# Kernel tuning notes

Measured on AMD Instinct MI355X. Metric: run time of the kernel, lower is better.

## Reference

```python
import jax, jax.numpy as jnp
import numpy as np

B, T, C, E = 16, 1024, 256, 512
NUM_CENTER = [512, 256, 128]
NUM_NNS = [16, 32, 64]
BN_EPS = 1e-5


def _fps(pts, K):
    # farthest point sampling, deterministic start at index 0. pts: [B,N,3] -> [B,K] int32
    N = pts.shape[1]
    def one(p):
        def step(carry, _):
            d, cur = carry
            dist = jnp.sum((p - p[cur]) ** 2, axis=-1)
            d = jnp.minimum(d, dist)
            nxt = jnp.argmax(d).astype(jnp.int32)
            return (d, nxt), cur
        init = (jnp.full((N,), jnp.inf, p.dtype), jnp.int32(0))
        _, idxs = jax.lax.scan(step, init, None, length=K)
        return idxs
    return jax.vmap(one)(pts)


def _knn(q, t, k):
    # k nearest neighbors of each query q [B,Tq,3] among targets t [B,Tt,3] -> [B,Tq,k]
    d2 = (jnp.sum(q * q, -1)[:, :, None] + jnp.sum(t * t, -1)[:, None, :]
          - 2.0 * jnp.einsum('bqc,btc->bqt', q, t))
    _, idx = jax.lax.top_k(-d2, k)
    return idx


def _gather(x, idx):
    # x [B,N,C], idx [B,M] -> [B,M,C]
    return jax.vmap(lambda xb, ib: xb[ib])(x, idx)


def _knn_gather(x, idx):
    # x [B,N,C], idx [B,M,K] -> [B,M,K,C]
    return jax.vmap(lambda xb, ib: xb[ib])(x, idx)


def _bn(x, g, b):
    # training-mode BatchNorm1d over leading (batch) dim of [N,C]
    m = jnp.mean(x, axis=0)
    v = jnp.mean((x - m) ** 2, axis=0)
    return (x - m) * jax.lax.rsqrt(v + BN_EPS) * g + b


def reference(tokens, centers, lrfs, wq, wkv, mlp_w1, mlp_b1, mlp_w2, mlp_b2,
              bn1_g, bn1_b, bn2_g, bn2_b, att_w1, att_b1, att_w2, att_b2,
              emb_w, emb_b, embn_g, embn_b):
    Bq, Tt, Cd = tokens.shape
    centers_target = centers
    lrfs_target = lrfs.reshape(Bq, Tt, 9)
    tokens_target = tokens
    T_target = Tt
    for i in range(len(NUM_CENTER)):
        Tq = NUM_CENTER[i]
        k = NUM_NNS[i]
        rep_idx = _fps(centers_target, Tq)                      # [B,Tq]
        centers_query = _gather(centers_target, rep_idx)        # [B,Tq,3]
        lrfs_query = _gather(lrfs_target, rep_idx)              # [B,Tq,9]
        tokens_query = _gather(tokens_target, rep_idx)          # [B,Tq,C]
        nn_idx = _knn(centers_query, centers_target, k)         # [B,Tq,k]
        skip = tokens_query.reshape(Bq * Tq, Cd)
        if i > 0:
            t = jnp.concatenate([tokens_query, tokens_target], axis=1)
            t = _bn(t.reshape(Bq * (Tq + T_target), Cd), bn1_g[i], bn1_b[i])
            t = t.reshape(Bq, Tq + T_target, Cd)
            tokens_query, tokens_target = t[:, :Tq, :], t[:, Tq:, :]
        Q = tokens_query @ wq[i]                                # [B,Tq,C]
        KV = tokens_target @ wkv[i]                             # [B,Tt,2C]
        Kf, Vf = KV[..., :Cd], KV[..., Cd:]
        Kn = _knn_gather(Kf, nn_idx).reshape(Bq * Tq, k, Cd)
        Vn = _knn_gather(Vf, nn_idx).reshape(Bq * Tq, k, Cd)
        Qf = Q.reshape(Bq * Tq, Cd)
        # vector self-attention: elementwise Q-K diff -> MLP -> softmax over neighbors
        diff = Qf[:, None, :] - Kn                              # [B*Tq,k,C]
        sim = jax.nn.relu(diff @ att_w1[i] + att_b1[i]) @ att_w2[i] + att_b2[i]
        A = jax.nn.softmax(sim, axis=1)
        tq = jnp.sum(A * Vn, axis=1)                            # [B*Tq,C]
        tq = tq + skip
        skip2 = tq
        tq = _bn(tq, bn2_g[i], bn2_b[i])
        tq = jax.nn.relu(tq @ mlp_w1[i] + mlp_b1[i]) @ mlp_w2[i] + mlp_b2[i]
        tq = tq + skip2
        T_target = Tq
        centers_target = centers_query
        lrfs_target = lrfs_query
        tokens_target = tq.reshape(Bq, Tq, Cd)
    g = jnp.mean(tokens_target, axis=1)                         # [B,C]
    g = jax.nn.relu(_bn(g @ emb_w + emb_b, embn_g, embn_b))     # [B,E]
    # ksparse: keep top-64 activations per row
    vals, _ = jax.lax.top_k(g, 64)
    thr = vals[:, -1:]
    g = jnp.where(g >= thr, g, 0.0)
    n = jnp.maximum(jnp.linalg.norm(g, axis=1, keepdims=True), 1e-12)
    return g / n


def setup_inputs() -> dict:
    key = jax.random.key(0)
    ks = jax.random.split(key, 10)
    s = 0.05
    return {
        'tokens': jax.random.normal(ks[0], (B, T, C), jnp.float32),
        'centers': jax.random.normal(ks[1], (B, T, 3), jnp.float32),
        'lrfs': jax.random.normal(ks[2], (B, T, 3, 3), jnp.float32),
        'wq': jax.random.normal(ks[3], (3, C, C), jnp.float32) * s,
        'wkv': jax.random.normal(ks[4], (3, C, 2 * C), jnp.float32) * s,
        'mlp_w1': jax.random.normal(ks[5], (3, C, 2 * C), jnp.float32) * s,
        'mlp_b1': jnp.zeros((3, 2 * C), jnp.float32),
        'mlp_w2': jax.random.normal(ks[6], (3, 2 * C, C), jnp.float32) * s,
        'mlp_b2': jnp.zeros((3, C), jnp.float32),
        'bn1_g': jnp.ones((3, C), jnp.float32),
        'bn1_b': jnp.zeros((3, C), jnp.float32),
        'bn2_g': jnp.ones((3, C), jnp.float32),
        'bn2_b': jnp.zeros((3, C), jnp.float32),
        'att_w1': jax.random.normal(ks[7], (3, C, C), jnp.float32) * s,
        'att_b1': jnp.zeros((3, C), jnp.float32),
        'att_w2': jax.random.normal(ks[8], (3, C, C), jnp.float32) * s,
        'att_b2': jnp.zeros((3, C), jnp.float32),
        'emb_w': jax.random.normal(ks[9], (C, E), jnp.float32) * s,
        'emb_b': jnp.zeros((E,), jnp.float32),
        'embn_g': jnp.ones((E,), jnp.float32),
        'embn_b': jnp.zeros((E,), jnp.float32),
    }
```

## Files before the change

### kernel.cpp

```cpp
#include <hip/hip_runtime.h>
#include <cstdint>
#include <cmath>

static constexpr int BB = 16;
static constexpr int TT0 = 1024;
static constexpr int CC = 256;
static constexpr int EE = 512;

typedef __bf16 bf16x8 __attribute__((ext_vector_type(8)));
typedef float  f32x4  __attribute__((ext_vector_type(4)));

template <int NPL>
__device__ void fps_body(float4* sp, const float* __restrict__ ctr,
                         int Tt, int Ksel, int* __restrict__ rep,
                         int b, int lane)
{
  const float* base = ctr + (size_t)b * Tt * 3;
  float x[NPL], y[NPL], z[NPL], d[NPL];
  #pragma unroll
  for (int j = 0; j < NPL; ++j) {
    int idx = lane * NPL + j;
    x[j] = base[idx * 3 + 0];
    y[j] = base[idx * 3 + 1];
    z[j] = base[idx * 3 + 2];
    d[j] = INFINITY;
    sp[idx] = make_float4(x[j], y[j], z[j], 0.f);
  }
  int cur = 0;
  for (int s = 0; s < Ksel; ++s) {
    if (lane == 0) rep[b * Ksel + s] = cur;
    float4 cpt = sp[cur];
    unsigned long long key = 0ull;
    #pragma unroll
    for (int j = 0; j < NPL; ++j) {
      float dx = __fsub_rn(x[j], cpt.x);
      float dy = __fsub_rn(y[j], cpt.y);
      float dz = __fsub_rn(z[j], cpt.z);
      float dist = __fadd_rn(__fadd_rn(__fmul_rn(dx, dx), __fmul_rn(dy, dy)),
                             __fmul_rn(dz, dz));
      float nd = fminf(d[j], dist);
      d[j] = nd;
      unsigned long long kj =
          ((unsigned long long)__float_as_uint(nd) << 32) |
          (unsigned)(0xFFFFFFFFu - (unsigned)(lane * NPL + j));
      key = (kj > key) ? kj : key;
    }
    float ld = __uint_as_float((unsigned)(key >> 32));
    float rm = ld;
    {
      int t;
      t = __builtin_amdgcn_mov_dpp(__float_as_int(rm), 0x121, 0xf, 0xf, false);
      rm = fmaxf(rm, __int_as_float(t));
      t = __builtin_amdgcn_mov_dpp(__float_as_int(rm), 0x122, 0xf, 0xf, false);
      rm = fmaxf(rm, __int_as_float(t));
      t = __builtin_amdgcn_mov_dpp(__float_as_int(rm), 0x124, 0xf, 0xf, false);
      rm = fmaxf(rm, __int_as_float(t));
      t = __builtin_amdgcn_mov_dpp(__float_as_int(rm), 0x128, 0xf, 0xf, false);
      rm = fmaxf(rm, __int_as_float(t));
    }
    float r0 = __uint_as_float((unsigned)__builtin_amdgcn_readlane(__float_as_int(rm), 0));
    float r1 = __uint_as_float((unsigned)__builtin_amdgcn_readlane(__float_as_int(rm), 16));
    float r2 = __uint_as_float((unsigned)__builtin_amdgcn_readlane(__float_as_int(rm), 32));
    float r3 = __uint_as_float((unsigned)__builtin_amdgcn_readlane(__float_as_int(rm), 48));
    float gm = fmaxf(fmaxf(r0, r1), fmaxf(r2, r3));
    unsigned long long mask = __ballot(ld == gm);
    int wl = __ffsll(mask) - 1;
    unsigned lowkey = (unsigned)__builtin_amdgcn_readlane((int)(unsigned)key, wl);
    cur = (int)(0xFFFFFFFFu - lowkey);
  }
}

template <int NPL2>
__global__ __launch_bounds__(256) void knn_wave_kernel(
    const float* __restrict__ cq, const float* __restrict__ ct,
    int Tq, int Tt, int Kn, int* __restrict__ nn)
{
  int wid = threadIdx.x >> 6, lane = threadIdx.x & 63;
  int r = blockIdx.x * 4 + wid;
  int b = r / Tq;
  const float* tb = ct + (size_t)b * Tt * 3;
  float qx = cq[(size_t)r * 3 + 0];
  float qy = cq[(size_t)r * 3 + 1];
  float qz = cq[(size_t)r * 3 + 2];
  float sq = __fadd_rn(__fadd_rn(__fmul_rn(qx, qx), __fmul_rn(qy, qy)),
                       __fmul_rn(qz, qz));
  unsigned long long key[NPL2];
  #pragma unroll
  for (int j = 0; j < NPL2; ++j) {
    int t = lane * NPL2 + j;
    float tx = tb[t * 3 + 0], ty = tb[t * 3 + 1], tz = tb[t * 3 + 2];
    float st = __fadd_rn(__fadd_rn(__fmul_rn(tx, tx), __fmul_rn(ty, ty)),
                         __fmul_rn(tz, tz));
    float dot = __fadd_rn(__fadd_rn(__fmul_rn(qx, tx), __fmul_rn(qy, ty)),
                          __fmul_rn(qz, tz));
    float d2 = __fsub_rn(__fadd_rn(sq, st), __fmul_rn(2.0f, dot));
    unsigned ub = __float_as_uint(d2);
    ub ^= (ub >> 31) ? 0xFFFFFFFFu : 0x80000000u;
    key[j] = ((unsigned long long)ub << 32) | (unsigned)t;
  }
  for (int k = 0; k < Kn; ++k) {
    unsigned long long lmin = ~0ull;
    #pragma unroll
    for (int j = 0; j < NPL2; ++j) lmin = (key[j] < lmin) ? key[j] : lmin;
    unsigned md = (unsigned)(lmin >> 32);
    unsigned rm = md;
    {
      unsigned t;
      t = (unsigned)__builtin_amdgcn_mov_dpp((int)rm, 0x121, 0xf, 0xf, false);
      rm = (t < rm) ? t : rm;
      t = (unsigned)__builtin_amdgcn_mov_dpp((int)rm, 0x122, 0xf, 0xf, false);
      rm = (t < rm) ? t : rm;
      t = (unsigned)__builtin_amdgcn_mov_dpp((int)rm, 0x124, 0xf, 0xf, false);
      rm = (t < rm) ? t : rm;
      t = (unsigned)__builtin_amdgcn_mov_dpp((int)rm, 0x128, 0xf, 0xf, false);
      rm = (t < rm) ? t : rm;
    }
    unsigned r0 = (unsigned)__builtin_amdgcn_readlane((int)rm, 0);
    unsigned r1 = (unsigned)__builtin_amdgcn_readlane((int)rm, 16);
    unsigned r2 = (unsigned)__builtin_amdgcn_readlane((int)rm, 32);
    unsigned r3 = (unsigned)__builtin_amdgcn_readlane((int)rm, 48);
    unsigned g01 = (r0 < r1) ? r0 : r1;
    unsigned g23 = (r2 < r3) ? r2 : r3;
    unsigned gmin = (g01 < g23) ? g01 : g23;
    unsigned long long mask = __ballot(md == gmin);
    int wl = __ffsll(mask) - 1;
    int wt = __builtin_amdgcn_readlane((int)(unsigned)lmin, wl);
    if (lane == 0) nn[(size_t)r * Kn + k] = wt;
    #pragma unroll
    for (int j = 0; j < NPL2; ++j)
      if (lane * NPL2 + j == wt) key[j] = ~0ull;
  }
}

__global__ void gather_rows_kernel(
    const float* __restrict__ src, const int* __restrict__ idx,
    float* __restrict__ dst, int Tq, int Tt, int D, int total)
{
  int i = blockIdx.x * blockDim.x + threadIdx.x;
  if (i >= total) return;
  int d = i % D;
  int q = (i / D) % Tq;
  int b = i / (D * Tq);
  int s = idx[b * Tq + q];
  dst[i] = src[((size_t)b * Tt + s) * D + d];
}

__global__ __launch_bounds__(256) void bn_stats_kernel(
    const float* __restrict__ x1, int R1, const float* __restrict__ x2, int R2,
    float* __restrict__ part, int nch)
{
  int c = threadIdx.x;
  int chunk = blockIdx.x;
  int R = R1 + R2;
  int per = (R + nch - 1) / nch;
  int r0 = chunk * per;
  int r1 = min(r0 + per, R);
  float s = 0.f, ss = 0.f;
  for (int r = r0; r < r1; ++r) {
    float v = (r < R1) ? x1[(size_t)r * 256 + c] : x2[(size_t)(r - R1) * 256 + c];
    s += v;
    ss = fmaf(v, v, ss);
  }
  part[(size_t)chunk * 512 + c] = s;
  part[(size_t)chunk * 512 + 256 + c] = ss;
}

__global__ __launch_bounds__(256) void bn_finalize_kernel(
    const float* __restrict__ part, int nch, int R,
    float* __restrict__ mean, float* __restrict__ rstd)
{
  int c = threadIdx.x;
  float s = 0.f, ss = 0.f;
  for (int k = 0; k < nch; ++k) {
    s += part[(size_t)k * 512 + c];
    ss += part[(size_t)k * 512 + 256 + c];
  }
  float m = s / (float)R;
  float v = ss / (float)R - m * m;
  if (v < 0.f) v = 0.f;
  mean[c] = m;
  rstd[c] = rsqrtf(v + 1e-5f);
}

__global__ __launch_bounds__(256) void gemm_kernel(
    const float* __restrict__ A, int lda,
    const float* __restrict__ W, int ldw,
    const float* __restrict__ bias, const float* __restrict__ resid,
    float* __restrict__ out, int M, int N, int K, int relu)
{
  __shared__ float As[32][68];
  __shared__ float Bs[32][68];
  int bm = blockIdx.y * 64;
  int bn = blockIdx.x * 64;
  int tid = threadIdx.x;
  int tx = tid & 15, ty = tid >> 4;
  int arow = tid >> 3;
  int ak = (tid & 7) * 4;
  int wk = tid >> 4;
  int wn = (tid & 15) * 4;
  float acc[4][4] = {{0.f}};
  for (int k0 = 0; k0 < K; k0 += 32) {
    #pragma unroll
    for (int h = 0; h < 2; ++h) {
      int row = bm + arow + h * 32;
      float4 a = (row < M)
          ? *(const float4*)&A[(size_t)row * lda + k0 + ak]
          : make_float4(0.f, 0.f, 0.f, 0.f);
      As[ak + 0][arow + h * 32] = a.x;
      As[ak + 1][arow + h * 32] = a.y;
      As[ak + 2][arow + h * 32] = a.z;
      As[ak + 3][arow + h * 32] = a.w;
    }
    #pragma unroll
    for (int h = 0; h < 2; ++h) {
      int krow = k0 + wk + h * 16;
      *(float4*)&Bs[wk + h * 16][wn] =
          *(const float4*)&W[(size_t)krow * ldw + bn + wn];
    }
    __syncthreads();
    #pragma unroll
    for (int k = 0; k < 32; ++k) {
      float4 a = *(const float4*)&As[k][ty * 4];
      float4 b = *(const float4*)&Bs[k][tx * 4];
      float av[4] = {a.x, a.y, a.z, a.w};
      float bv[4] = {b.x, b.y, b.z, b.w};
      #pragma unroll
      for (int i = 0; i < 4; ++i)
        #pragma unroll
        for (int j = 0; j < 4; ++j)
          acc[i][j] = fmaf(av[i], bv[j], acc[i][j]);
    }
    __syncthreads();
  }
  #pragma unroll
  for (int i = 0; i < 4; ++i) {
    int m = bm + ty * 4 + i;
    if (m >= M) continue;
    #pragma unroll
    for (int j = 0; j < 4; ++j) {
      int n = bn + tx * 4 + j;
      float v = acc[i][j];
      if (bias) v += bias[n];
      if (relu) v = fmaxf(v, 0.f);
      if (resid) v += resid[(size_t)m * N + n];
      out[(size_t)m * N + n] = v;
    }
  }
}

__global__ __launch_bounds__(256) void gemm_fold_split_kernel(
    const float* __restrict__ A, int lda,
    const float* __restrict__ W, int ldw,
    __bf16* __restrict__ hi, __bf16* __restrict__ lo, int M, int N, int K)
{
  __shared__ float As[32][68];
  __shared__ float Bs[32][68];
  int bm = blockIdx.y * 64;
  int bn = blockIdx.x * 64;
  int tid = threadIdx.x;
  int tx = tid & 15, ty = tid >> 4;
  int arow = tid >> 3;
  int ak = (tid & 7) * 4;
  int wk = tid >> 4;
  int wn = (tid & 15) * 4;
  float acc[4][4] = {{0.f}};
  for (int k0 = 0; k0 < K; k0 += 32) {
    #pragma unroll
    for (int h = 0; h < 2; ++h) {
      int row = bm + arow + h * 32;
      float4 a = *(const float4*)&A[(size_t)row * lda + k0 + ak];
      As[ak + 0][arow + h * 32] = a.x;
      As[ak + 1][arow + h * 32] = a.y;
      As[ak + 2][arow + h * 32] = a.z;
      As[ak + 3][arow + h * 32] = a.w;
    }
    #pragma unroll
    for (int h = 0; h < 2; ++h) {
      int krow = k0 + wk + h * 16;
      *(float4*)&Bs[wk + h * 16][wn] =
          *(const float4*)&W[(size_t)krow * ldw + bn + wn];
    }
    __syncthreads();
    #pragma unroll
    for (int k = 0; k < 32; ++k) {
      float4 a = *(const float4*)&As[k][ty * 4];
      float4 b = *(const float4*)&Bs[k][tx * 4];
      float av[4] = {a.x, a.y, a.z, a.w};
      float bv[4] = {b.x, b.y, b.z, b.w};
      #pragma unroll
      for (int i = 0; i < 4; ++i)
        #pragma unroll
        for (int j = 0; j < 4; ++j)
          acc[i][j] = fmaf(av[i], bv[j], acc[i][j]);
    }
    __syncthreads();
  }
  #pragma unroll
  for (int i = 0; i < 4; ++i) {
    int m = bm + ty * 4 + i;
    #pragma unroll
    for (int j = 0; j < 4; ++j) {
      int n = bn + tx * 4 + j;
      float v = acc[i][j];
      __bf16 h = (__bf16)v;
      hi[(size_t)n * K + m] = h;
      lo[(size_t)n * K + m] = (__bf16)(v - (float)h);
    }
  }
}

__global__ void splitT_kernel(
    const float* __restrict__ src, int ldw, int K, int N,
    __bf16* __restrict__ hi, __bf16* __restrict__ lo, int total)
{
  int i = blockIdx.x * blockDim.x + threadIdx.x;
  if (i >= total) return;
  int n = i / K;
  int k = i - n * K;
  float v = src[(size_t)k * ldw + n];
  __bf16 h = (__bf16)v;
  hi[i] = h;
  lo[i] = (__bf16)(v - (float)h);
}

__global__ __launch_bounds__(256) void split_w2_kernel(
    const float* __restrict__ w2, __bf16* __restrict__ hi,
    __bf16* __restrict__ lo)
{
  int i = blockIdx.x * 256 + threadIdx.x;
  int s = i >> 16;
  int e = i & 65535;
  int cp = e >> 8;
  int cc = e & 255;
  float v = w2[((size_t)s << 16) + cc * 256 + cp];
  __bf16 h = (__bf16)v;
  hi[i] = h;
  lo[i] = (__bf16)(v - (float)h);
}

template <int NPL>
__global__ __launch_bounds__(256) void gemm_mfma_kernel(
    const float* __restrict__ A, int lda,
    const __bf16* __restrict__ WThi, const __bf16* __restrict__ WTlo,
    const float* __restrict__ bias, const float* __restrict__ resid,
    float* __restrict__ out, int M, int N, int K, int relu,
    const float* __restrict__ bnm, const float* __restrict__ bnr,
    const float* __restrict__ bng, const float* __restrict__ bnb,
    int nbx,
    const float* __restrict__ fps_ctr, int fps_Tt, int fps_Ksel,
    int* __restrict__ fps_rep)
{
  __shared__ __align__(16) float As[128 * 36];
  if ((int)blockIdx.x >= nbx) {
    if (fps_rep == nullptr || (int)blockIdx.y >= BB) return;
    if ((int)threadIdx.x >= 64) return;
    fps_body<NPL>((float4*)As, fps_ctr, fps_Tt, fps_Ksel, fps_rep,
                  blockIdx.y, threadIdx.x);
    return;
  }
  int bm = blockIdx.y * 128;
  int bn = blockIdx.x * 64;
  int tid = threadIdx.x;
  int w = tid >> 6, lane = tid & 63;
  int jl = lane & 15;
  int kg = lane >> 4;

  f32x4 acc[2][4];
  #pragma unroll
  for (int mt = 0; mt < 2; ++mt)
    #pragma unroll
    for (int nt = 0; nt < 4; ++nt) acc[mt][nt] = (f32x4){0.f, 0.f, 0.f, 0.f};

  for (int k0 = 0; k0 < K; k0 += 32) {
    #pragma unroll
    for (int f = 0; f < 4; ++f) {
      int fi = tid + f * 256;
      int row = fi >> 3, c4 = fi & 7;
      float4 v = *(const float4*)&A[(size_t)(bm + row) * lda + k0 + c4 * 4];
      if (bnm) {
        int kk = k0 + c4 * 4;
        float4 m4 = *(const float4*)&bnm[kk];
        float4 r4 = *(const float4*)&bnr[kk];
        float4 g4 = *(const float4*)&bng[kk];
        float4 b4 = *(const float4*)&bnb[kk];
        v.x = (v.x - m4.x) * r4.x * g4.x + b4.x;
        v.y = (v.y - m4.y) * r4.y * g4.y + b4.y;
        v.z = (v.z - m4.z) * r4.z * g4.z + b4.z;
        v.w = (v.w - m4.w) * r4.w * g4.w + b4.w;
      }
      *(float4*)&As[row * 36 + c4 * 4] = v;
    }
    __syncthreads();
    bf16x8 ahi[2], alo[2];
    #pragma unroll
    for (int mt = 0; mt < 2; ++mt) {
      int row = (w * 2 + mt) * 16 + jl;
      float4 a0 = *(const float4*)&As[row * 36 + kg * 8];
      float4 a1 = *(const float4*)&As[row * 36 + kg * 8 + 4];
      float hv[8] = {a0.x, a0.y, a0.z, a0.w, a1.x, a1.y, a1.z, a1.w};
      #pragma unroll
      for (int i = 0; i < 8; ++i) {
        __bf16 t0 = (__bf16)hv[i];
        ahi[mt][i] = t0;
        alo[mt][i] = (__bf16)(hv[i] - (float)t0);
      }
    }
    #pragma unroll
    for (int nt = 0; nt < 4; ++nt) {
      size_t boff = (size_t)(bn + nt * 16 + jl) * K + k0 + kg * 8;
      bf16x8 bhi = *(const bf16x8*)(WThi + boff);
      bf16x8 blo = *(const bf16x8*)(WTlo + boff);
      #pragma unroll
      for (int mt = 0; mt < 2; ++mt) {
        acc[mt][nt] = __builtin_amdgcn_mfma_f32_16x16x32_bf16(alo[mt], bhi, acc[mt][nt], 0, 0, 0);
        acc[mt][nt] = __builtin_amdgcn_mfma_f32_16x16x32_bf16(ahi[mt], blo, acc[mt][nt], 0, 0, 0);
        acc[mt][nt] = __builtin_amdgcn_mfma_f32_16x16x32_bf16(ahi[mt], bhi, acc[mt][nt], 0, 0, 0);
      }
    }
    __syncthreads();
  }
  #pragma unroll
  for (int mt = 0; mt < 2; ++mt)
    #pragma unroll
    for (int nt = 0; nt < 4; ++nt)
      #pragma unroll
      for (int qi = 0; qi < 4; ++qi) {
        int m = bm + (w * 2 + mt) * 16 + kg * 4 + qi;
        int n = bn + nt * 16 + jl;
        float v = acc[mt][nt][qi];
        if (bias) v += bias[n];
        if (relu) v = fmaxf(v, 0.f);
        if (resid) v += resid[(size_t)m * N + n];
        out[(size_t)m * N + n] = v;
      }
}

template <int KN, int NPL>
__global__ __launch_bounds__(256, 2) void attn5_kernel(
    const float* __restrict__ Qw, const float* __restrict__ KV,
    const int* __restrict__ nn,
    const float* __restrict__ b1, const __bf16* __restrict__ w2Thi,
    const __bf16* __restrict__ w2Tlo, const float* __restrict__ b2,
    const float* __restrict__ skip, float* __restrict__ out, int Tq, int Tt,
    int nbx,
    const float* __restrict__ fps_ctr, int fps_Tt, int fps_Ksel,
    int* __restrict__ fps_rep)
{
  constexpr int G  = 128 / KN;
  constexpr int GC = 64 / KN;
  constexpr int LD = 260;
  __shared__ __align__(16) float sim[64 * LD];
  __shared__ int nns[128];
  if ((int)blockIdx.x >= nbx) {
    if (fps_rep == nullptr) return;
    int fb = blockIdx.x - nbx;
    if (fb >= BB) return;
    if ((int)threadIdx.x >= 64) return;
    fps_body<NPL>((float4*)sim, fps_ctr, fps_Tt, fps_Ksel, fps_rep,
                  fb, threadIdx.x);
    return;
  }
  int r0 = blockIdx.x * G;
  int b = r0 / Tq;
  int tid = threadIdx.x;
  if (tid < 128) nns[tid] = nn[(size_t)r0 * KN + tid];
  __syncthreads();

  int w = tid >> 6, lane = tid & 63;
  int jl = lane & 15;
  int kg = lane >> 4;
  int nt0 = w * 4;
  const float* kvb = KV + (size_t)b * Tt * 512;

  f32x4 acc[8][4];
  #pragma unroll
  for (int m = 0; m < 8; ++m)
    #pragma unroll
    for (int n = 0; n < 4; ++n) acc[m][n] = (f32x4){0.f, 0.f, 0.f, 0.f};

  const float* qp[8];
  const float* kp[8];
  #pragma unroll
  for (int mt = 0; mt < 8; ++mt) {
    int jr = mt * 16 + jl;
    qp[mt] = Qw + (size_t)(r0 + jr / KN) * 256;
    kp[mt] = kvb + (size_t)nns[jr] * 512;
  }

  #pragma unroll
  for (int ks = 0; ks < 8; ++ks) {
    int c0 = ks * 32 + kg * 8;
    float4 b1a = *(const float4*)(b1 + c0);
    float4 b1b = *(const float4*)(b1 + c0 + 4);
    bf16x8 ahi[8], alo[8];
    #pragma unroll
    for (int mt = 0; mt < 8; ++mt) {
      float4 qa = *(const float4*)(qp[mt] + c0);
      float4 qb = *(const float4*)(qp[mt] + c0 + 4);
      float4 ka = *(const float4*)(kp[mt] + c0);
      float4 kb = *(const float4*)(kp[mt] + c0 + 4);
      float h[8];
      h[0] = fmaxf(qa.x - ka.x + b1a.x, 0.f);
      h[1] = fmaxf(qa.y - ka.y + b1a.y, 0.f);
      h[2] = fmaxf(qa.z - ka.z + b1a.z, 0.f);
      h[3] = fmaxf(qa.w - ka.w + b1a.w, 0.f);
      h[4] = fmaxf(qb.x - kb.x + b1b.x, 0.f);
      h[5] = fmaxf(qb.y - kb.y + b1b.y, 0.f);
      h[6] = fmaxf(qb.z - kb.z + b1b.z, 0.f);
      h[7] = fmaxf(qb.w - kb.w + b1b.w, 0.f);
      #pragma unroll
      for (int i = 0; i < 8; ++i) {
        __bf16 t0 = (__bf16)h[i];
        ahi[mt][i] = t0;
        alo[mt][i] = (__bf16)(h[i] - (float)t0);
      }
    }
    #pragma unroll
    for (int t = 0; t < 4; ++t) {
      size_t boff = (size_t)((nt0 + t) * 16 + jl) * 256 + c0;
      bf16x8 bhi = *(const bf16x8*)(w2Thi + boff);
      bf16x8 blo = *(const bf16x8*)(w2Tlo + boff);
      #pragma unroll
      for (int mt = 0; mt < 8; ++mt) {
        acc[mt][t] = __builtin_amdgcn_mfma_f32_16x16x32_bf16(alo[mt], bhi, acc[mt][t], 0, 0, 0);
        acc[mt][t] = __builtin_amdgcn_mfma_f32_16x16x32_bf16(ahi[mt], blo, acc[mt][t], 0, 0, 0);
        acc[mt][t] = __builtin_amdgcn_mfma_f32_16x16x32_bf16(ahi[mt], bhi, acc[mt][t], 0, 0, 0);
      }
    }
  }

  int c = tid;
  float bb2 = b2[c];
  const float* vbb = kvb + 256;
  #pragma unroll
  for (int ch = 0; ch < 2; ++ch) {
    if (ch) __syncthreads();
    #pragma unroll
    for (int m2 = 0; m2 < 4; ++m2) {
      int mt = ch * 4 + m2;
      #pragma unroll
      for (int t = 0; t < 4; ++t)
        #pragma unroll
        for (int qi = 0; qi < 4; ++qi)
          sim[(m2 * 16 + kg * 4 + qi) * LD + (nt0 + t) * 16 + jl] = acc[mt][t][qi];
    }
    __syncthreads();
    #pragma unroll
    for (int gg = 0; gg < GC; ++gg) {
      int jb_l = gg * KN;
      int jb_g = ch * 64 + gg * KN;
      float m = -INFINITY;
      #pragma unroll 8
      for (int jj = 0; jj < KN; ++jj)
        m = fmaxf(m, sim[(jb_l + jj) * LD + c] + bb2);
      float ssum = 0.f, o = 0.f;
      #pragma unroll 8
      for (int jj = 0; jj < KN; ++jj) {
        float e = expf(sim[(jb_l + jj) * LD + c] + bb2 - m);
        ssum += e;
        o = fmaf(e, vbb[(size_t)nns[jb_g + jj] * 512 + c], o);
      }
      int r = r0 + ch * GC + gg;
      out[(size_t)r * 256 + c] = o / ssum + skip[(size_t)r * 256 + c];
    }
  }
}

__global__ void gmean_kernel(const float* __restrict__ tok,
                             float* __restrict__ out, int Tt)
{
  int i = blockIdx.x * blockDim.x + threadIdx.x;
  if (i >= BB * CC) return;
  int b = i >> 8;
  int c = i & 255;
  float s = 0.f;
  for (int t = 0; t < Tt; ++t) s += tok[((size_t)b * Tt + t) * 256 + c];
  out[i] = s / (float)Tt;
}

__global__ void embbn_kernel(const float* __restrict__ x,
                             const float* __restrict__ g,
                             const float* __restrict__ bta,
                             float* __restrict__ y)
{
  int e = blockIdx.x * blockDim.x + threadIdx.x;
  if (e >= EE) return;
  float s = 0.f;
  for (int r = 0; r < BB; ++r) s += x[r * EE + e];
  float m = s / (float)BB;
  float vs = 0.f;
  for (int r = 0; r < BB; ++r) {
    float d = x[r * EE + e] - m;
    vs = fmaf(d, d, vs);
  }
  float rs = rsqrtf(vs / (float)BB + 1e-5f);
  for (int r = 0; r < BB; ++r) {
    float val = (x[r * EE + e] - m) * rs * g[e] + bta[e];
    y[r * EE + e] = fmaxf(val, 0.f);
  }
}

__global__ __launch_bounds__(256) void topk_norm_kernel(
    const float* __restrict__ gin, float* __restrict__ out)
{
  int b = blockIdx.x, tid = threadIdx.x, lane = tid & 63, wid = tid >> 6;
  __shared__ float vals[512];
  __shared__ float wv[4];
  __shared__ int wi[4];
  __shared__ float sh;
  float g0 = gin[b * 512 + tid];
  float g1 = gin[b * 512 + 256 + tid];
  vals[tid] = g0;
  vals[256 + tid] = g1;
  __syncthreads();
  for (int it = 0; it < 64; ++it) {
    float v = vals[tid];
    int ix = tid;
    float u = vals[256 + tid];
    if (u > v) { v = u; ix = 256 + tid; }
    #pragma unroll
    for (int off = 32; off > 0; off >>= 1) {
      float ov = __shfl_down(v, off);
      int oi = __shfl_down(ix, off);
      if (ov > v || (ov == v && oi < ix)) { v = ov; ix = oi; }
    }
    if (lane == 0) { wv[wid] = v; wi[wid] = ix; }
    __syncthreads();
    if (tid == 0) {
      float bv = wv[0]; int bi = wi[0];
      for (int w = 1; w < 4; ++w)
        if (wv[w] > bv || (wv[w] == bv && wi[w] < bi)) { bv = wv[w]; bi = wi[w]; }
      vals[bi] = -INFINITY;
      sh = bv;
    }
    __syncthreads();
  }
  float thr = sh;
  float m0 = (g0 >= thr) ? g0 : 0.f;
  float m1 = (g1 >= thr) ? g1 : 0.f;
  float ss = m0 * m0 + m1 * m1;
  #pragma unroll
  for (int off = 32; off > 0; off >>= 1) ss += __shfl_down(ss, off);
  if (lane == 0) wv[wid] = ss;
  __syncthreads();
  if (tid == 0) {
    float t = wv[0] + wv[1] + wv[2] + wv[3];
    sh = fmaxf(sqrtf(t), 1e-12f);
  }
  __syncthreads();
  float n = sh;
  out[b * 512 + tid] = m0 / n;
  out[b * 512 + 256 + tid] = m1 / n;
}

extern "C" void kernel_launch(void* const* d_in, const int* in_sizes, int n_in,
                              void* d_out, int out_size, void* d_ws, size_t ws_size,
                              hipStream_t stream)
{
  const float* tokens  = (const float*)d_in[0];
  const float* centers = (const float*)d_in[1];
  const float* wq      = (const float*)d_in[3];
  const float* wkv     = (const float*)d_in[4];
  const float* mlp_w1  = (const float*)d_in[5];
  const float* mlp_b1  = (const float*)d_in[6];
  const float* mlp_w2  = (const float*)d_in[7];
  const float* mlp_b2  = (const float*)d_in[8];
  const float* bn1_g   = (const float*)d_in[9];
  const float* bn1_b   = (const float*)d_in[10];
  const float* bn2_g   = (const float*)d_in[11];
  const float* bn2_b   = (const float*)d_in[12];
  const float* att_w1  = (const float*)d_in[13];
  const float* att_b1  = (const float*)d_in[14];
  const float* att_w2  = (const float*)d_in[15];
  const float* att_b2  = (const float*)d_in[16];
  const float* emb_w   = (const float*)d_in[17];
  const float* emb_b   = (const float*)d_in[18];
  const float* embn_g  = (const float*)d_in[19];
  const float* embn_b  = (const float*)d_in[20];
  (void)in_sizes; (void)n_in; (void)out_size; (void)ws_size;

  char* ws = (char*)d_ws;
  size_t off = 0;
  auto alloc = [&](size_t bytes) -> void* {
    void* p = ws + off;
    off += (bytes + 255) & ~(size_t)255;
    return p;
  };
  const size_t tokMax  = (size_t)BB * 512 * CC * 4;
  float* tokA     = (float*)alloc(tokMax);
  float* tokB     = (float*)alloc(tokMax);
  float* ctrA     = (float*)alloc((size_t)BB * 512 * 3 * 4);
  float* ctrB     = (float*)alloc((size_t)BB * 256 * 3 * 4);
  float* ctrC     = (float*)alloc((size_t)BB * 128 * 3 * 4);
  float* tokq_raw = (float*)alloc(tokMax);
  float* Qw1      = (float*)alloc(tokMax);
  float* KVbuf    = (float*)alloc((size_t)BB * 1024 * 512 * 4);
  float* tq1      = (float*)alloc(tokMax);
  float* mlph     = (float*)alloc((size_t)BB * 512 * 512 * 4);
  __bf16* w2Thi   = (__bf16*)alloc((size_t)3 * CC * CC * 2);
  __bf16* w2Tlo   = (__bf16*)alloc((size_t)3 * CC * CC * 2);
  __bf16* wfqThi  = (__bf16*)alloc((size_t)3 * CC * CC * 2);
  __bf16* wfqTlo  = (__bf16*)alloc((size_t)3 * CC * CC * 2);
  __bf16* wkvThi  = (__bf16*)alloc((size_t)3 * 512 * CC * 2);
  __bf16* wkvTlo  = (__bf16*)alloc((size_t)3 * 512 * CC * 2);
  __bf16* w1Thi   = (__bf16*)alloc((size_t)3 * CC * 512 * 2);
  __bf16* w1Tlo   = (__bf16*)alloc((size_t)3 * CC * 512 * 2);
  __bf16* wm2Thi  = (__bf16*)alloc((size_t)3 * 512 * CC * 2);
  __bf16* wm2Tlo  = (__bf16*)alloc((size_t)3 * 512 * CC * 2);
  int*   rep0     = (int*)alloc((size_t)BB * 512 * 4);
  int*   rep1     = (int*)alloc((size_t)BB * 256 * 4);
  int*   rep2     = (int*)alloc((size_t)BB * 128 * 4);
  int*   nnb      = (int*)alloc((size_t)BB * 512 * 64 * 4);
  float* bnpart   = (float*)alloc((size_t)64 * 512 * 4);
  float* bn1mean  = (float*)alloc(256 * 4);
  float* bn1rstd  = (float*)alloc(256 * 4);
  float* bn2mean  = (float*)alloc(256 * 4);
  float* bn2rstd  = (float*)alloc(256 * 4);
  float* gmeanb   = (float*)alloc((size_t)BB * CC * 4);
  float* gembb    = (float*)alloc((size_t)BB * EE * 4);
  float* grelub   = (float*)alloc((size_t)BB * EE * 4);

  const int NC[3] = {512, 256, 128};
  const int NN[3] = {16, 32, 64};
  int* reps[3] = {rep0, rep1, rep2};
  float* ctrq[3] = {ctrA, ctrB, ctrC};

  for (int i = 0; i < 3; ++i) {
    int t1 = CC * CC;
    gemm_fold_split_kernel<<<dim3(4, 4), 256, 0, stream>>>(
        wq + (size_t)i * CC * CC, CC, att_w1 + (size_t)i * CC * CC, CC,
        wfqThi + (size_t)i * t1, wfqTlo + (size_t)i * t1, CC, CC, CC);
    gemm_fold_split_kernel<<<dim3(4, 4), 256, 0, stream>>>(
        wkv + (size_t)i * CC * 512, 512, att_w1 + (size_t)i * CC * CC, CC,
        wkvThi + (size_t)i * 512 * CC, wkvTlo + (size_t)i * 512 * CC, CC, CC, CC);
    splitT_kernel<<<(t1 + 255) / 256, 256, 0, stream>>>(
        wkv + (size_t)i * CC * 512 + CC, 512, CC, CC,
        wkvThi + (size_t)i * 512 * CC + t1, wkvTlo + (size_t)i * 512 * CC + t1, t1);
    int t2 = CC * 512;
    splitT_kernel<<<(t2 + 255) / 256, 256, 0, stream>>>(
        mlp_w1 + (size_t)i * t2, 512, CC, 512,
        w1Thi + (size_t)i * t2, w1Tlo + (size_t)i * t2, t2);
    splitT_kernel<<<(t2 + 255) / 256, 256, 0, stream>>>(
        mlp_w2 + (size_t)i * t2, CC, 512, CC,
        wm2Thi + (size_t)i * t2, wm2Tlo + (size_t)i * t2, t2);
  }
  split_w2_kernel<<<3 * 65536 / 256, 256, 0, stream>>>(att_w2, w2Thi, w2Tlo);

  const float* cur_tok = tokens;
  const float* cur_ctr = centers;
  int curTt = TT0;
  float* tok_bufs[2] = {tokA, tokB};

  for (int i = 0; i < 3; ++i) {
    int Tq = NC[i], Kn = NN[i], Tt = curTt;
    float* ctr_q = ctrq[i];
    float* tok_next = tok_bufs[i & 1];
    int M = BB * Tq;
    int Mt = BB * Tt;
    int* rep = reps[i];

    const float *b1m = nullptr, *b1r = nullptr, *b1g = nullptr, *b1b = nullptr;

    if (i == 0) {
      gemm_mfma_kernel<16><<<dim3(512 / 64 + 1, Mt / 128), 256, 0, stream>>>(
          tokens, CC, wkvThi, wkvTlo, nullptr, nullptr, KVbuf,
          Mt, 512, CC, 0, nullptr, nullptr, nullptr, nullptr,
          512 / 64, centers, 1024, 512, rep0);
    }

    {
      int tot = BB * Tq * 3;
      gather_rows_kernel<<<(tot + 255) / 256, 256, 0, stream>>>(
          cur_ctr, rep, ctr_q, Tq, Tt, 3, tot);
    }
    {
      int tot = M * CC;
      gather_rows_kernel<<<(tot + 255) / 256, 256, 0, stream>>>(
          cur_tok, rep, tokq_raw, Tq, Tt, CC, tot);
    }
    if (Tt == 1024)
      knn_wave_kernel<16><<<M / 4, 256, 0, stream>>>(ctr_q, cur_ctr, Tq, Tt, Kn, nnb);
    else if (Tt == 512)
      knn_wave_kernel<8><<<M / 4, 256, 0, stream>>>(ctr_q, cur_ctr, Tq, Tt, Kn, nnb);
    else
      knn_wave_kernel<4><<<M / 4, 256, 0, stream>>>(ctr_q, cur_ctr, Tq, Tt, Kn, nnb);

    if (i > 0) {
      bn_stats_kernel<<<64, 256, 0, stream>>>(tokq_raw, M, cur_tok, Mt, bnpart, 64);
      bn_finalize_kernel<<<1, 256, 0, stream>>>(bnpart, 64, M + Mt, bn1mean, bn1rstd);
      b1m = bn1mean; b1r = bn1rstd; b1g = bn1_g + i * CC; b1b = bn1_b + i * CC;
      gemm_mfma_kernel<4><<<dim3(512 / 64, Mt / 128), 256, 0, stream>>>(
          cur_tok, CC, wkvThi + (size_t)i * 512 * CC, wkvTlo + (size_t)i * 512 * CC,
          nullptr, nullptr, KVbuf, Mt, 512, CC, 0, b1m, b1r, b1g, b1b,
          512 / 64, nullptr, 0, 0, nullptr);
    }

    gemm_mfma_kernel<4><<<dim3(CC / 64, M / 128), 256, 0, stream>>>(
        tokq_raw, CC, wfqThi + (size_t)i * CC * CC, wfqTlo + (size_t)i * CC * CC,
        nullptr, nullptr, Qw1, M, CC, CC, 0, b1m, b1r, b1g, b1b,
        CC / 64, nullptr, 0, 0, nullptr);

    if (Kn == 16)
      attn5_kernel<16, 8><<<dim3(M / 8 + 16), 256, 0, stream>>>(
          Qw1, KVbuf, nnb, att_b1 + i * CC,
          w2Thi + (size_t)i * CC * CC, w2Tlo + (size_t)i * CC * CC,
          att_b2 + i * CC, tokq_raw, tq1, Tq, Tt,
          M / 8, ctrA, 512, 256, rep1);
    else if (Kn == 32)
      attn5_kernel<32, 4><<<dim3(M / 4 + 16), 256, 0, stream>>>(
          Qw1, KVbuf, nnb, att_b1 + i * CC,
          w2Thi + (size_t)i * CC * CC, w2Tlo + (size_t)i * CC * CC,
          att_b2 + i * CC, tokq_raw, tq1, Tq, Tt,
          M / 4, ctrB, 256, 128, rep2);
    else
      attn5_kernel<64, 4><<<dim3(M / 2), 256, 0, stream>>>(
          Qw1, KVbuf, nnb, att_b1 + i * CC,
          w2Thi + (size_t)i * CC * CC, w2Tlo + (size_t)i * CC * CC,
          att_b2 + i * CC, tokq_raw, tq1, Tq, Tt,
          M / 2, nullptr, 0, 0, nullptr);

    bn_stats_kernel<<<64, 256, 0, stream>>>(tq1, M, tq1, 0, bnpart, 64);
    bn_finalize_kernel<<<1, 256, 0, stream>>>(bnpart, 64, M, bn2mean, bn2rstd);
    gemm_mfma_kernel<4><<<dim3(512 / 64, M / 128), 256, 0, stream>>>(
        tq1, CC, w1Thi + (size_t)i * CC * 512, w1Tlo + (size_t)i * CC * 512,
        mlp_b1 + i * 512, nullptr, mlph, M, 512, CC, 1,
        bn2mean, bn2rstd, bn2_g + i * CC, bn2_b + i * CC,
        512 / 64, nullptr, 0, 0, nullptr);
    gemm_mfma_kernel<4><<<dim3(CC / 64, M / 128), 256, 0, stream>>>(
        mlph, 512, wm2Thi + (size_t)i * 512 * CC, wm2Tlo + (size_t)i * 512 * CC,
        mlp_b2 + i * CC, tq1, tok_next, M, CC, 512, 0,
        nullptr, nullptr, nullptr, nullptr,
        CC / 64, nullptr, 0, 0, nullptr);

    cur_tok = tok_next;
    cur_ctr = ctr_q;
    curTt = Tq;
  }

  gmean_kernel<<<(BB * CC + 255) / 256, 256, 0, stream>>>(cur_tok, gmeanb, curTt);
  gemm_kernel<<<dim3(EE / 64, 1), 256, 0, stream>>>(
      gmeanb, CC, emb_w, EE, emb_b, nullptr, gembb, BB, EE, CC, 0);
  embbn_kernel<<<2, 256, 0, stream>>>(gembb, embn_g, embn_b, grelub);
  topk_norm_kernel<<<BB, 256, 0, stream>>>(grelub, (float*)d_out);
}
```

Baseline: 1.638 ms.

## Fuse stage-0 query projection into KV GEMM and relocate FPS side blocks

```diff
diff --git a/kernel.cpp b/kernel.cpp
--- a/kernel.cpp
+++ b/kernel.cpp
@@ -435,31 +435,20 @@
       }
 }
 
-template <int KN, int NPL>
+template <int KN>
 __global__ __launch_bounds__(256, 2) void attn5_kernel(
-    const float* __restrict__ Qw, const float* __restrict__ KV,
+    const float* __restrict__ Qw, const float* __restrict__ KV, int kvld,
+    const int* __restrict__ qrep,
     const int* __restrict__ nn,
     const float* __restrict__ b1, const __bf16* __restrict__ w2Thi,
     const __bf16* __restrict__ w2Tlo, const float* __restrict__ b2,
-    const float* __restrict__ skip, float* __restrict__ out, int Tq, int Tt,
-    int nbx,
-    const float* __restrict__ fps_ctr, int fps_Tt, int fps_Ksel,
-    int* __restrict__ fps_rep)
+    const float* __restrict__ skip, float* __restrict__ out, int Tq, int Tt)
 {
   constexpr int G  = 128 / KN;
   constexpr int GC = 64 / KN;
   constexpr int LD = 260;
   __shared__ __align__(16) float sim[64 * LD];
   __shared__ int nns[128];
-  if ((int)blockIdx.x >= nbx) {
-    if (fps_rep == nullptr) return;
-    int fb = blockIdx.x - nbx;
-    if (fb >= BB) return;
-    if ((int)threadIdx.x >= 64) return;
-    fps_body<NPL>((float4*)sim, fps_ctr, fps_Tt, fps_Ksel, fps_rep,
-                  fb, threadIdx.x);
-    return;
-  }
   int r0 = blockIdx.x * G;
   int b = r0 / Tq;
   int tid = threadIdx.x;
@@ -470,7 +459,7 @@
   int jl = lane & 15;
   int kg = lane >> 4;
   int nt0 = w * 4;
-  const float* kvb = KV + (size_t)b * Tt * 512;
+  const float* kvb = KV + (size_t)b * Tt * kvld;
 
   f32x4 acc[8][4];
   #pragma unroll
@@ -483,8 +472,10 @@
   #pragma unroll
   for (int mt = 0; mt < 8; ++mt) {
     int jr = mt * 16 + jl;
-    qp[mt] = Qw + (size_t)(r0 + jr / KN) * 256;
-    kp[mt] = kvb + (size_t)nns[jr] * 512;
+    int rq = r0 + jr / KN;
+    qp[mt] = qrep ? (kvb + (size_t)qrep[rq] * kvld + 512)
+                  : (Qw + (size_t)rq * 256);
+    kp[mt] = kvb + (size_t)nns[jr] * kvld;
   }
 
   #pragma unroll
@@ -558,7 +549,7 @@
       for (int jj = 0; jj < KN; ++jj) {
         float e = expf(sim[(jb_l + jj) * LD + c] + bb2 - m);
         ssum += e;
-        o = fmaf(e, vbb[(size_t)nns[jb_g + jj] * 512 + c], o);
+        o = fmaf(e, vbb[(size_t)nns[jb_g + jj] * kvld + c], o);
       }
       int r = r0 + ch * GC + gg;
       out[(size_t)r * 256 + c] = o / ssum + skip[(size_t)r * 256 + c];
@@ -694,13 +685,15 @@
   float* ctrC     = (float*)alloc((size_t)BB * 128 * 3 * 4);
   float* tokq_raw = (float*)alloc(tokMax);
   float* Qw1      = (float*)alloc(tokMax);
-  float* KVbuf    = (float*)alloc((size_t)BB * 1024 * 512 * 4);
+  float* KVbuf    = (float*)alloc((size_t)BB * 1024 * 768 * 4);
   float* tq1      = (float*)alloc(tokMax);
   float* mlph     = (float*)alloc((size_t)BB * 512 * 512 * 4);
   __bf16* w2Thi   = (__bf16*)alloc((size_t)3 * CC * CC * 2);
   __bf16* w2Tlo   = (__bf16*)alloc((size_t)3 * CC * CC * 2);
   __bf16* wfqThi  = (__bf16*)alloc((size_t)3 * CC * CC * 2);
   __bf16* wfqTlo  = (__bf16*)alloc((size_t)3 * CC * CC * 2);
+  __bf16* wkvqThi = (__bf16*)alloc((size_t)768 * CC * 2);
+  __bf16* wkvqTlo = (__bf16*)alloc((size_t)768 * CC * 2);
   __bf16* wkvThi  = (__bf16*)alloc((size_t)3 * 512 * CC * 2);
   __bf16* wkvTlo  = (__bf16*)alloc((size_t)3 * 512 * CC * 2);
   __bf16* w1Thi   = (__bf16*)alloc((size_t)3 * CC * 512 * 2);
@@ -725,7 +718,16 @@
   int* reps[3] = {rep0, rep1, rep2};
   float* ctrq[3] = {ctrA, ctrB, ctrC};
 
-  for (int i = 0; i < 3; ++i) {
+  {
+    int t1 = CC * CC;
+    gemm_fold_split_kernel<<<dim3(4, 4), 256, 0, stream>>>(
+        wkv, 512, att_w1, CC, wkvqThi, wkvqTlo, CC, CC, CC);
+    splitT_kernel<<<(t1 + 255) / 256, 256, 0, stream>>>(
+        wkv + CC, 512, CC, CC, wkvqThi + t1, wkvqTlo + t1, t1);
+    gemm_fold_split_kernel<<<dim3(4, 4), 256, 0, stream>>>(
+        wq, CC, att_w1, CC, wkvqThi + 2 * t1, wkvqTlo + 2 * t1, CC, CC, CC);
+  }
+  for (int i = 1; i < 3; ++i) {
     int t1 = CC * CC;
     gemm_fold_split_kernel<<<dim3(4, 4), 256, 0, stream>>>(
         wq + (size_t)i * CC * CC, CC, att_w1 + (size_t)i * CC * CC, CC,
@@ -736,6 +738,8 @@
     splitT_kernel<<<(t1 + 255) / 256, 256, 0, stream>>>(
         wkv + (size_t)i * CC * 512 + CC, 512, CC, CC,
         wkvThi + (size_t)i * 512 * CC + t1, wkvTlo + (size_t)i * 512 * CC + t1, t1);
+  }
+  for (int i = 0; i < 3; ++i) {
     int t2 = CC * 512;
     splitT_kernel<<<(t2 + 255) / 256, 256, 0, stream>>>(
         mlp_w1 + (size_t)i * t2, 512, CC, 512,
@@ -758,14 +762,15 @@
     int M = BB * Tq;
     int Mt = BB * Tt;
     int* rep = reps[i];
+    int kvld = (i == 0) ? 768 : 512;
 
     const float *b1m = nullptr, *b1r = nullptr, *b1g = nullptr, *b1b = nullptr;
 
     if (i == 0) {
-      gemm_mfma_kernel<16><<<dim3(512 / 64 + 1, Mt / 128), 256, 0, stream>>>(
-          tokens, CC, wkvThi, wkvTlo, nullptr, nullptr, KVbuf,
-          Mt, 512, CC, 0, nullptr, nullptr, nullptr, nullptr,
-          512 / 64, centers, 1024, 512, rep0);
+      gemm_mfma_kernel<16><<<dim3(768 / 64 + 1, Mt / 128), 256, 0, stream>>>(
+          tokens, CC, wkvqThi, wkvqTlo, nullptr, nullptr, KVbuf,
+          Mt, 768, CC, 0, nullptr, nullptr, nullptr, nullptr,
+          768 / 64, centers, 1024, 512, rep0);
     }
 
     {
@@ -789,43 +794,53 @@
       bn_stats_kernel<<<64, 256, 0, stream>>>(tokq_raw, M, cur_tok, Mt, bnpart, 64);
       bn_finalize_kernel<<<1, 256, 0, stream>>>(bnpart, 64, M + Mt, bn1mean, bn1rstd);
       b1m = bn1mean; b1r = bn1rstd; b1g = bn1_g + i * CC; b1b = bn1_b + i * CC;
-      gemm_mfma_kernel<4><<<dim3(512 / 64, Mt / 128), 256, 0, stream>>>(
-          cur_tok, CC, wkvThi + (size_t)i * 512 * CC, wkvTlo + (size_t)i * 512 * CC,
-          nullptr, nullptr, KVbuf, Mt, 512, CC, 0, b1m, b1r, b1g, b1b,
-          512 / 64, nullptr, 0, 0, nullptr);
-    }
-
-    gemm_mfma_kernel<4><<<dim3(CC / 64, M / 128), 256, 0, stream>>>(
-        tokq_raw, CC, wfqThi + (size_t)i * CC * CC, wfqTlo + (size_t)i * CC * CC,
-        nullptr, nullptr, Qw1, M, CC, CC, 0, b1m, b1r, b1g, b1b,
-        CC / 64, nullptr, 0, 0, nullptr);
-
+      if (i == 1)
+        gemm_mfma_kernel<4><<<dim3(512 / 64 + 1, Mt / 128), 256, 0, stream>>>(
+            cur_tok, CC, wkvThi + (size_t)i * 512 * CC, wkvTlo + (size_t)i * 512 * CC,
+            nullptr, nullptr, KVbuf, Mt, 512, CC, 0, b1m, b1r, b1g, b1b,
+            512 / 64, ctrB, 256, 128, rep2);
+      else
+        gemm_mfma_kernel<4><<<dim3(512 / 64, Mt / 128), 256, 0, stream>>>(
+            cur_tok, CC, wkvThi + (size_t)i * 512 * CC, wkvTlo + (size_t)i * 512 * CC,
+            nullptr, nullptr, KVbuf, Mt, 512, CC, 0, b1m, b1r, b1g, b1b,
+            512 / 64, nullptr, 0, 0, nullptr);
+      gemm_mfma_kernel<4><<<dim3(CC / 64, M / 128), 256, 0, stream>>>(
+          tokq_raw, CC, wfqThi + (size_t)i * CC * CC, wfqTlo + (size_t)i * CC * CC,
+          nullptr, nullptr, Qw1, M, CC, CC, 0, b1m, b1r, b1g, b1b,
+          CC / 64, nullptr, 0, 0, nullptr);
+    }
+
+    const int* qrep = (i == 0) ? rep0 : nullptr;
     if (Kn == 16)
-      attn5_kernel<16, 8><<<dim3(M / 8 + 16), 256, 0, stream>>>(
-          Qw1, KVbuf, nnb, att_b1 + i * CC,
+      attn5_kernel<16><<<dim3(M / 8), 256, 0, stream>>>(
+          Qw1, KVbuf, kvld, qrep, nnb, att_b1 + i * CC,
           w2Thi + (size_t)i * CC * CC, w2Tlo + (size_t)i * CC * CC,
-          att_b2 + i * CC, tokq_raw, tq1, Tq, Tt,
-          M / 8, ctrA, 512, 256, rep1);
+          att_b2 + i * CC, tokq_raw, tq1, Tq, Tt);
     else if (Kn == 32)
-      attn5_kernel<32, 4><<<dim3(M / 4 + 16), 256, 0, stream>>>(
-          Qw1, KVbuf, nnb, att_b1 + i * CC,
+      attn5_kernel<32><<<dim3(M / 4), 256, 0, stream>>>(
+          Qw1, KVbuf, kvld, qrep, nnb, att_b1 + i * CC,
           w2Thi + (size_t)i * CC * CC, w2Tlo + (size_t)i * CC * CC,
-          att_b2 + i * CC, tokq_raw, tq1, Tq, Tt,
-          M / 4, ctrB, 256, 128, rep2);
+          att_b2 + i * CC, tokq_raw, tq1, Tq, Tt);
     else
-      attn5_kernel<64, 4><<<dim3(M / 2), 256, 0, stream>>>(
-          Qw1, KVbuf, nnb, att_b1 + i * CC,
+      attn5_kernel<64><<<dim3(M / 2), 256, 0, stream>>>(
+          Qw1, KVbuf, kvld, qrep, nnb, att_b1 + i * CC,
           w2Thi + (size_t)i * CC * CC, w2Tlo + (size_t)i * CC * CC,
-          att_b2 + i * CC, tokq_raw, tq1, Tq, Tt,
-          M / 2, nullptr, 0, 0, nullptr);
+          att_b2 + i * CC, tokq_raw, tq1, Tq, Tt);
 
     bn_stats_kernel<<<64, 256, 0, stream>>>(tq1, M, tq1, 0, bnpart, 64);
     bn_finalize_kernel<<<1, 256, 0, stream>>>(bnpart, 64, M, bn2mean, bn2rstd);
-    gemm_mfma_kernel<4><<<dim3(512 / 64, M / 128), 256, 0, stream>>>(
-        tq1, CC, w1Thi + (size_t)i * CC * 512, w1Tlo + (size_t)i * CC * 512,
-        mlp_b1 + i * 512, nullptr, mlph, M, 512, CC, 1,
-        bn2mean, bn2rstd, bn2_g + i * CC, bn2_b + i * CC,
-        512 / 64, nullptr, 0, 0, nullptr);
+    if (i == 0)
+      gemm_mfma_kernel<8><<<dim3(512 / 64 + 1, M / 128), 256, 0, stream>>>(
+          tq1, CC, w1Thi + (size_t)i * CC * 512, w1Tlo + (size_t)i * CC * 512,
+          mlp_b1 + i * 512, nullptr, mlph, M, 512, CC, 1,
+          bn2mean, bn2rstd, bn2_g + i * CC, bn2_b + i * CC,
+          512 / 64, ctrA, 512, 256, rep1);
+    else
+      gemm_mfma_kernel<4><<<dim3(512 / 64, M / 128), 256, 0, stream>>>(
+          tq1, CC, w1Thi + (size_t)i * CC * 512, w1Tlo + (size_t)i * CC * 512,
+          mlp_b1 + i * 512, nullptr, mlph, M, 512, CC, 1,
+          bn2mean, bn2rstd, bn2_g + i * CC, bn2_b + i * CC,
+          512 / 64, nullptr, 0, 0, nullptr);
     gemm_mfma_kernel<4><<<dim3(CC / 64, M / 128), 256, 0, stream>>>(
         mlph, 512, wm2Thi + (size_t)i * 512 * CC, wm2Tlo + (size_t)i * 512 * CC,
         mlp_b2 + i * CC, tq1, tok_next, M, CC, 512, 0,
```

After: 1.640 ms, median of 2. Within noise of the previous version (+0.2%).
